# Performance work log

Measured on AMD Instinct MI355X. Metric: run time of the kernel, lower is better.

## Reference

```python
import jax, jax.numpy as jnp
import numpy as np

TINY = 1e-6
MIN_DEG, MAX_DEG = 0, 16

# 3x21 icosahedral basis used for the background (non-diag) IPE
P = jnp.asarray(np.array([
    0.8506508, 0.0, 0.5257311, 0.809017, 0.5, 0.309017, 0.5257311, 0.8506508, 0.0,
    1.0, 0.0, 0.0, 0.809017, 0.5, -0.309017, 0.8506508, 0.0, -0.5257311, 0.309017,
    0.809017, -0.5, 0.0, 0.5257311, -0.8506508, 0.5, 0.309017, -0.809017, 0.0, 1.0,
    0.0, -0.5257311, 0.8506508, 0.0, -0.309017, 0.809017, -0.5, 0.0, 0.5257311,
    0.8506508, -0.309017, 0.809017, 0.5, 0.309017, 0.809017, 0.5, 0.5, 0.309017,
    0.809017, 0.5, -0.309017, 0.809017, 0.0, 0.0, 1.0, -0.5, 0.309017, 0.809017,
    -0.809017, 0.5, 0.309017, -0.809017, 0.5, -0.309017], dtype=np.float32).reshape(3, 21))


def setup_inputs() -> dict:
    key = jax.random.key(0)
    k1, k2, k3, k4, k5 = jax.random.split(key, 5)
    N, Ns = 2048, 64
    ray_o = jax.random.normal(k1, (N, 3), dtype=jnp.float32)
    ray_d = jax.random.normal(k2, (N, 3), dtype=jnp.float32)
    fg_z_vals = jnp.sort(jax.random.uniform(k3, (N, Ns + 1), minval=0.1, maxval=5.0), axis=-1)
    bg_z_vals = jnp.sort(jax.random.uniform(k4, (N, Ns + 1), minval=1.0, maxval=50.0), axis=-1)
    radii = jax.random.uniform(k5, (N, 1), minval=0.005, maxval=0.02)
    return {"ray_o": ray_o, "ray_d": ray_d, "fg_z_vals": fg_z_vals,
            "bg_z_vals": bg_z_vals, "radii": radii}


def _frustum_moments(t0, t1, base_radius):
    mu = (t0 + t1) / 2.0
    hw = (t1 - t0) / 2.0
    denom = 3.0 * mu ** 2 + hw ** 2
    t_mean = mu + 2.0 * mu * hw ** 2 / denom
    t_var = hw ** 2 / 3.0 - (4.0 / 15.0) * (hw ** 4 * (12.0 * mu ** 2 - hw ** 2) / denom ** 2)
    r_var = base_radius ** 2 * (mu ** 2 / 4.0 + (5.0 / 12.0) * hw ** 2 - (4.0 / 15.0) * hw ** 4 / denom)
    return t_mean, t_var, r_var


def cast_rays_diag(t_vals, origins, directions, radii):
    t_mean, t_var, r_var = _frustum_moments(t_vals[..., :-1], t_vals[..., 1:], radii)
    d = directions[..., None, :]                      # [N,1,3]
    mean = d * t_mean[..., None]                      # [N,Ns,3]
    d_mag_sq = jnp.maximum(1e-8, jnp.sum(d ** 2, axis=-1, keepdims=True))
    d_outer_diag = d ** 2
    null_outer_diag = 1.0 - d_outer_diag / d_mag_sq
    cov_diag = t_var[..., None] * d_outer_diag + r_var[..., None] * null_outer_diag
    return mean + origins[..., None, :], cov_diag


def cast_rays_full(t_vals, origins, directions, radii):
    t_mean, t_var, r_var = _frustum_moments(t_vals[..., :-1], t_vals[..., 1:], radii)
    d = directions[..., None, :]                      # [N,1,3]
    mean = d * t_mean[..., None]                      # [N,Ns,3]
    d_mag_sq = jnp.maximum(1e-8, jnp.sum(d ** 2, axis=-1, keepdims=True))
    d_outer = d[..., :, None] * d[..., None, :]       # [N,1,3,3]
    eye = jnp.eye(3, dtype=d.dtype)
    null_outer = eye - d[..., :, None] * (d / d_mag_sq)[..., None, :]
    cov = t_var[..., None, None] * d_outer + r_var[..., None, None] * null_outer
    return mean + origins[..., None, :], cov          # [N,Ns,3], [N,Ns,3,3]


def _contract_point(x):
    n = jnp.linalg.norm(x) + TINY
    return (2.0 - 1.0 / n) * (x / n)


def contract_gaussian(mean, cov_full):
    N, Ns = mean.shape[0], mean.shape[1]
    flat = mean.reshape(-1, 3)
    J = jax.vmap(jax.jacfwd(_contract_point))(flat).reshape(N, Ns, 3, 3)
    n = jnp.linalg.norm(mean, axis=-1, keepdims=True) + TINY
    mean_c = (2.0 - 1.0 / n) * (mean / n)
    cov_c = jnp.einsum('nsij,nsjk,nslk->nsil', J, cov_full, J)
    return mean_c, cov_c


def expected_sin(x, x_var):
    return jnp.exp(-0.5 * x_var) * jnp.sin(x)


def ipe_diag(x, x_cov_diag, min_deg, max_deg):
    scales = 2.0 ** jnp.arange(min_deg, max_deg, dtype=x.dtype)   # [L]
    N, Ns = x.shape[0], x.shape[1]
    y = (x[..., None, :] * scales[:, None]).reshape(N, Ns, -1)                 # [N,Ns,L*3]
    y_var = (x_cov_diag[..., None, :] * (scales ** 2)[:, None]).reshape(N, Ns, -1)
    return expected_sin(jnp.concatenate([y, y + 0.5 * jnp.pi], axis=-1),
                        jnp.concatenate([y_var, y_var], axis=-1))


def ipe_full(x, x_cov, min_deg, max_deg):
    y = jnp.matmul(x, P)                                                        # [N,Ns,21]
    y_var = jnp.einsum('nsab,bk,ak->nsk', x_cov, P, P)                          # [N,Ns,21]
    scales = 2.0 ** jnp.arange(min_deg, max_deg, dtype=x.dtype)
    N, Ns = x.shape[0], x.shape[1]
    y = (y[..., None, :] * scales[:, None]).reshape(N, Ns, -1)                  # [N,Ns,L*21]
    y_var = (y_var[..., None, :] * (scales ** 2)[:, None]).reshape(N, Ns, -1)
    return expected_sin(jnp.concatenate([y, y + 0.5 * jnp.pi], axis=-1),
                        jnp.concatenate([y_var, y_var], axis=-1))


def reference(ray_o, ray_d, fg_z_vals, bg_z_vals, radii):
    # foreground: diagonal-cov cone cast + diagonal IPE  -> [N,Ns,96]
    fg_mean, fg_cov_diag = cast_rays_diag(fg_z_vals, ray_o, ray_d, radii)
    enc_fg = ipe_diag(fg_mean, fg_cov_diag, MIN_DEG, MAX_DEG)
    # background: full-cov cone cast + contraction Jacobian + basis IPE -> [N,Ns,672]
    bg_mean, bg_cov = cast_rays_full(bg_z_vals, ray_o, ray_d, radii)
    mean_c, cov_c = contract_gaussian(bg_mean, bg_cov)
    enc_bg = ipe_full(mean_c, cov_c, MIN_DEG, MAX_DEG)
    return jnp.concatenate([enc_fg, enc_bg], axis=-1)                            # [N,Ns,768]
```

## Files before the change

### kernel.cpp

```cpp
#include <hip/hip_runtime.h>
#include <math.h>

#define NS 64
#define INV2PI  0.15915494309189535f
#define NEGHL2E (-0.72134752044448170f)

__constant__ float c_P[63] = {
  0.8506508f, 0.0f, 0.5257311f, 0.809017f, 0.5f, 0.309017f, 0.5257311f,
  0.8506508f, 0.0f, 1.0f, 0.0f, 0.0f, 0.809017f, 0.5f, -0.309017f,
  0.8506508f, 0.0f, -0.5257311f, 0.309017f, 0.809017f, -0.5f,
  0.0f, 0.5257311f, -0.8506508f, 0.5f, 0.309017f, -0.809017f, 0.0f, 1.0f,
  0.0f, -0.5257311f, 0.8506508f, 0.0f, -0.309017f, 0.809017f, -0.5f, 0.0f,
  0.5257311f, 0.8506508f, -0.309017f, 0.809017f, 0.5f,
  0.309017f, 0.809017f, 0.5f, 0.5f, 0.309017f, 0.809017f, 0.5f, -0.309017f,
  0.809017f, 0.0f, 0.0f, 1.0f, -0.5f, 0.309017f, 0.809017f, -0.809017f,
  0.5f, 0.309017f, -0.809017f, 0.5f, -0.309017f
};

struct Moments { float t_mean, t_var, r_var; };

__device__ inline Moments frustum_moments(float t0, float t1, float radius) {
    float mu  = 0.5f * (t0 + t1);
    float hw  = 0.5f * (t1 - t0);
    float mu2 = mu * mu, hw2 = hw * hw;
    float denom = 3.0f * mu2 + hw2;
    float inv_d = 1.0f / denom;
    float hw4 = hw2 * hw2;
    Moments m;
    m.t_mean = mu + 2.0f * mu * hw2 * inv_d;
    m.t_var  = hw2 * (1.0f / 3.0f)
             - (4.0f / 15.0f) * (hw4 * (12.0f * mu2 - hw2) * inv_d * inv_d);
    m.r_var  = radius * radius *
               (0.25f * mu2 + (5.0f / 12.0f) * hw2 - (4.0f / 15.0f) * hw4 * inv_d);
    return m;
}

__global__ __launch_bounds__(256) void mipnerf_enc(
    const float* __restrict__ ray_o,
    const float* __restrict__ ray_d,
    const float* __restrict__ fgz,
    const float* __restrict__ bgz,
    const float* __restrict__ radii,
    float* __restrict__ out)
{
    const int n   = blockIdx.x;
    const int tid = threadIdx.x;

    __shared__ float sXV[NS * 50];
    __shared__ float sCore[NS * 11];

    const float ox = ray_o[3 * n + 0], oy = ray_o[3 * n + 1], oz = ray_o[3 * n + 2];
    const float dx = ray_d[3 * n + 0], dy = ray_d[3 * n + 1], dz = ray_d[3 * n + 2];
    const float rad = radii[n];
    const float dm = fmaxf(1e-8f, dx * dx + dy * dy + dz * dz);
    const float inv_dm = 1.0f / dm;

    if (tid < NS) {
        const int s = tid;
        {
            float t0 = fgz[(NS + 1) * n + s];
            float t1 = fgz[(NS + 1) * n + s + 1];
            Moments mm = frustum_moments(t0, t1, rad);
            float d3[3] = {dx, dy, dz};
            float o3[3] = {ox, oy, oz};
            #pragma unroll
            for (int i = 0; i < 3; ++i) {
                float m  = o3[i] + d3[i] * mm.t_mean;
                float dd = d3[i] * d3[i];
                float cd = mm.t_var * dd + mm.r_var * (1.0f - dd * inv_dm);
                sXV[s * 50 + 2 * (21 + i) + 0] = m  * INV2PI;
                sXV[s * 50 + 2 * (21 + i) + 1] = cd * NEGHL2E;
            }
        }
        {
            float t0 = bgz[(NS + 1) * n + s];
            float t1 = bgz[(NS + 1) * n + s + 1];
            Moments mm = frustum_moments(t0, t1, rad);
            float x0 = ox + dx * mm.t_mean;
            float x1 = oy + dy * mm.t_mean;
            float x2 = oz + dz * mm.t_mean;
            float a  = mm.t_var - mm.r_var * inv_dm;
            float rv = mm.r_var;
            float rn2 = x0 * x0 + x1 * x1 + x2 * x2;
            float rn  = sqrtf(rn2);
            float nn  = rn + 1e-6f;
            float inn = 1.0f / nn;
            float g   = (2.0f * nn - 1.0f) * inn * inn;
            float gp  = 2.0f * (1.0f - nn) * inn * inn * inn;
            float h   = gp / rn;
            float xd  = x0 * dx + x1 * dy + x2 * dz;
            float hxd = h * xd;
            float u0 = g * dx + hxd * x0;
            float u1 = g * dy + hxd * x1;
            float u2 = g * dz + hxd * x2;
            float w  = 2.0f * g * h + h * h * rn2;
            float* cr = &sCore[s * 11];
            cr[0] = x0; cr[1] = x1; cr[2] = x2;
            cr[3] = u0; cr[4] = u1; cr[5] = u2;
            cr[6] = g;  cr[7] = a;  cr[8] = rv * g * g; cr[9] = rv * w;
        }
    }
    __syncthreads();

    #pragma unroll
    for (int j = 0; j < 6; ++j) {
        int i = tid + 256 * j;
        if (i < 21 * NS) {
            int k = i >> 6;
            int s = i & (NS - 1);
            const float p0 = c_P[k], p1 = c_P[21 + k], p2 = c_P[42 + k];
            const float* cr = &sCore[s * 11];
            float x0 = cr[0], x1 = cr[1], x2 = cr[2];
            float u0 = cr[3], u1 = cr[4], u2 = cr[5];
            float g = cr[6], c1 = cr[7], c2 = cr[8], c3 = cr[9];
            float dpx = p0 * x0 + p1 * x1 + p2 * x2;
            float dpu = p0 * u0 + p1 * u1 + p2 * u2;
            float pp  = p0 * p0 + p1 * p1 + p2 * p2;
            float y   = g * dpx;
            float yv  = c1 * dpu * dpu + c2 * pp + c3 * dpx * dpx;
            sXV[s * 50 + 2 * k + 0] = y  * INV2PI;
            sXV[s * 50 + 2 * k + 1] = yv * NEGHL2E;
        }
    }
    __syncthreads();

    float4* __restrict__ outv = reinterpret_cast<float4*>(out) + (size_t)n * (NS * 768 / 4);
    for (int it = 0; it < 48; ++it) {
        int idx = tid + 256 * it;
        int s   = idx / 192;
        int c   = (idx - s * 192) * 4;
        int deg, src, srcLo, srcHi;
        float phq;
        if (c < 96) {
            int ph = (c >= 48) ? 1 : 0;
            int jj = c - 48 * ph;
            deg = jj / 3;
            src = 21 + (jj - 3 * deg);
            srcLo = 21; srcHi = 24;
            phq = 0.25f * (float)ph;
        } else {
            int local = c - 96;
            int ph = (local >= 336) ? 1 : 0;
            int jj = local - 336 * ph;
            deg = jj / 21;
            src = jj - 21 * deg;
            srcLo = 0; srcHi = 21;
            phq = 0.25f * (float)ph;
        }
        const float* rowXV = &sXV[s * 50];
        float vals[4];
        #pragma unroll
        for (int q = 0; q < 4; ++q) {
            float X = rowXV[2 * src + 0];
            float V = rowXV[2 * src + 1];
            float sf  = __int_as_float((127 + deg) << 23);
            float s2f = __int_as_float((127 + 2 * deg) << 23);
            float e = __builtin_amdgcn_exp2f(V * s2f);
            float r = __builtin_amdgcn_fractf(X * sf + phq);
            vals[q] = e * __builtin_amdgcn_sinf(r);
            if (++src == srcHi) { src = srcLo; ++deg; }
        }
        outv[idx] = make_float4(vals[0], vals[1], vals[2], vals[3]);
    }
}

extern "C" void kernel_launch(void* const* d_in, const int* in_sizes, int n_in,
                              void* d_out, int out_size, void* d_ws, size_t ws_size,
                              hipStream_t stream) {
    const float* ray_o = (const float*)d_in[0];
    const float* ray_d = (const float*)d_in[1];
    const float* fgz   = (const float*)d_in[2];
    const float* bgz   = (const float*)d_in[3];
    const float* radii = (const float*)d_in[4];
    float* out = (float*)d_out;
    const int N = in_sizes[0] / 3;
    mipnerf_enc<<<N, 256, 0, stream>>>(ray_o, ray_d, fgz, bgz, radii, out);
}
```

Measured before the change: 414.5 us.

## Precompute output descriptors in LDS, pair sin/cos work, use nontemporal stores

Builds a shared table of packed (scale exponent, source offset) descriptors so the output loop no longer does per-element index division and branching. Each thread now computes the sin and cos phase of four features together, reusing one exp2 and one LDS load per pair. It writes both results with nontemporal float4 stores, and launch bounds now request 4 blocks per CU. The intent is less integer and ALU overhead and less cache pollution from the large write stream, in exchange for extra LDS and a setup pass.

```diff
diff --git a/kernel.cpp b/kernel.cpp
--- a/kernel.cpp
+++ b/kernel.cpp
@@ -4,6 +4,8 @@
 #define NS 64
 #define INV2PI  0.15915494309189535f
 #define NEGHL2E (-0.72134752044448170f)
+
+typedef __attribute__((ext_vector_type(4))) float vfloat4;
 
 __constant__ float c_P[63] = {
   0.8506508f, 0.0f, 0.5257311f, 0.809017f, 0.5f, 0.309017f, 0.5257311f,
@@ -35,7 +37,7 @@
     return m;
 }
 
-__global__ __launch_bounds__(256) void mipnerf_enc(
+__global__ __launch_bounds__(256, 4) void mipnerf_enc(
     const float* __restrict__ ray_o,
     const float* __restrict__ ray_d,
     const float* __restrict__ fgz,
@@ -48,6 +50,7 @@
 
     __shared__ float sXV[NS * 50];
     __shared__ float sCore[NS * 11];
+    __shared__ unsigned int sDesc[384];
 
     const float ox = ray_o[3 * n + 0], oy = ray_o[3 * n + 1], oz = ray_o[3 * n + 2];
     const float dx = ray_d[3 * n + 0], dy = ray_d[3 * n + 1], dz = ray_d[3 * n + 2];
@@ -99,6 +102,13 @@
             cr[3] = u0; cr[4] = u1; cr[5] = u2;
             cr[6] = g;  cr[7] = a;  cr[8] = rv * g * g; cr[9] = rv * w;
         }
+    } else {
+        for (int e = tid - NS; e < 384; e += 256 - NS) {
+            int deg, src;
+            if (e < 48) { deg = e / 3;  src = 21 + (e - 3 * deg); }
+            else { int jj = e - 48; deg = jj / 21; src = jj - 21 * deg; }
+            sDesc[e] = ((unsigned)(127 + deg) << 23) | ((unsigned)src << 3);
+        }
     }
     __syncthreads();
 
@@ -124,43 +134,58 @@
     }
     __syncthreads();
 
-    float4* __restrict__ outv = reinterpret_cast<float4*>(out) + (size_t)n * (NS * 768 / 4);
-    for (int it = 0; it < 48; ++it) {
-        int idx = tid + 256 * it;
-        int s   = idx / 192;
-        int c   = (idx - s * 192) * 4;
-        int deg, src, srcLo, srcHi;
-        float phq;
-        if (c < 96) {
-            int ph = (c >= 48) ? 1 : 0;
-            int jj = c - 48 * ph;
-            deg = jj / 3;
-            src = 21 + (jj - 3 * deg);
-            srcLo = 21; srcHi = 24;
-            phq = 0.25f * (float)ph;
-        } else {
-            int local = c - 96;
-            int ph = (local >= 336) ? 1 : 0;
-            int jj = local - 336 * ph;
-            deg = jj / 21;
-            src = jj - 21 * deg;
-            srcLo = 0; srcHi = 21;
-            phq = 0.25f * (float)ph;
-        }
-        const float* rowXV = &sXV[s * 50];
-        float vals[4];
-        #pragma unroll
-        for (int q = 0; q < 4; ++q) {
-            float X = rowXV[2 * src + 0];
-            float V = rowXV[2 * src + 1];
-            float sf  = __int_as_float((127 + deg) << 23);
-            float s2f = __int_as_float((127 + 2 * deg) << 23);
-            float e = __builtin_amdgcn_exp2f(V * s2f);
-            float r = __builtin_amdgcn_fractf(X * sf + phq);
-            vals[q] = e * __builtin_amdgcn_sinf(r);
-            if (++src == srcHi) { src = srcLo; ++deg; }
-        }
-        outv[idx] = make_float4(vals[0], vals[1], vals[2], vals[3]);
+    float* __restrict__ outp = out + (size_t)n * (NS * 768);
+
+    for (int it = 0; it < 24; ++it) {
+        int p  = tid + 256 * it;
+        int s  = p / 96;
+        int j0 = (p - s * 96) << 2;
+        const uint4 w4 = *reinterpret_cast<const uint4*>(&sDesc[j0]);
+        const char* rowXV = reinterpret_cast<const char*>(&sXV[s * 50]);
+        const bool fg = (j0 < 48);
+
+        vfloat4 vs, vc;
+        {
+            unsigned w = w4.x;
+            float sf = __uint_as_float(w & 0xFF800000u);
+            float2 xv = *reinterpret_cast<const float2*>(rowXV + (w & 0xFFu));
+            float e  = __builtin_amdgcn_exp2f(xv.y * (sf * sf));
+            float xs = xv.x * sf;
+            vs.x = e * __builtin_amdgcn_sinf(__builtin_amdgcn_fractf(xs));
+            vc.x = e * __builtin_amdgcn_sinf(__builtin_amdgcn_fractf(xs + 0.25f));
+        }
+        {
+            unsigned w = w4.y;
+            float sf = __uint_as_float(w & 0xFF800000u);
+            float2 xv = *reinterpret_cast<const float2*>(rowXV + (w & 0xFFu));
+            float e  = __builtin_amdgcn_exp2f(xv.y * (sf * sf));
+            float xs = xv.x * sf;
+            vs.y = e * __builtin_amdgcn_sinf(__builtin_amdgcn_fractf(xs));
+            vc.y = e * __builtin_amdgcn_sinf(__builtin_amdgcn_fractf(xs + 0.25f));
+        }
+        {
+            unsigned w = w4.z;
+            float sf = __uint_as_float(w & 0xFF800000u);
+            float2 xv = *reinterpret_cast<const float2*>(rowXV + (w & 0xFFu));
+            float e  = __builtin_amdgcn_exp2f(xv.y * (sf * sf));
+            float xs = xv.x * sf;
+            vs.z = e * __builtin_amdgcn_sinf(__builtin_amdgcn_fractf(xs));
+            vc.z = e * __builtin_amdgcn_sinf(__builtin_amdgcn_fractf(xs + 0.25f));
+        }
+        {
+            unsigned w = w4.w;
+            float sf = __uint_as_float(w & 0xFF800000u);
+            float2 xv = *reinterpret_cast<const float2*>(rowXV + (w & 0xFFu));
+            float e  = __builtin_amdgcn_exp2f(xv.y * (sf * sf));
+            float xs = xv.x * sf;
+            vs.w = e * __builtin_amdgcn_sinf(__builtin_amdgcn_fractf(xs));
+            vc.w = e * __builtin_amdgcn_sinf(__builtin_amdgcn_fractf(xs + 0.25f));
+        }
+
+        float* o1 = outp + (s * 768 + (fg ? j0 : j0 + 48));
+        float* o2 = o1 + (fg ? 48 : 336);
+        __builtin_nontemporal_store(vs, reinterpret_cast<vfloat4*>(o1));
+        __builtin_nontemporal_store(vc, reinterpret_cast<vfloat4*>(o2));
     }
 }
 
```

Result: no change. 416.9 us (+0.6%).
